# Optimization experiments

Measured on AMD Instinct MI355X. Metric: run time of the kernel, lower is better.

The kernel has to match this reference:

```python
import jax, jax.numpy as jnp
import numpy as np

N, E = 50000, 800000
SD, VD = 128, 16        # node scalar / vector channels
ESD, EVD = 32, 1        # edge scalar / vector channels
LN_EPS = 1e-5
VN_EPS = 1e-8


def setup_inputs():
    key = jax.random.key(0)
    ks = jax.random.split(key, 24)
    g = lambda i, shape, scale=0.05: jax.random.normal(ks[i], shape, dtype=jnp.float32) * scale
    inp = dict(
        node_s=jax.random.normal(ks[0], (N, SD), dtype=jnp.float32),
        node_v=jax.random.normal(ks[1], (N, VD, 3), dtype=jnp.float32),
        edge_index=jax.random.randint(ks[2], (2, E), 0, N, dtype=jnp.int32),
        edge_s=jax.random.normal(ks[3], (E, ESD), dtype=jnp.float32),
        edge_v=jax.random.normal(ks[4], (E, EVD, 3), dtype=jnp.float32),
        # LayerNorm (scalar channel) params
        ln_g=jnp.ones((SD,), jnp.float32), ln_b=jnp.zeros((SD,), jnp.float32),
        # edge_gvp: (ESD,EVD) -> (SD,VD)
        wes=g(5, (SD, ESD)), bes=jnp.zeros((SD,), jnp.float32),
        wev=g(6, (VD * 3, EVD * 3)), bev=jnp.zeros((VD * 3,), jnp.float32),
        # node_gvp: (SD,VD) -> (SD,VD)
        wns=g(7, (SD, SD)), bns=jnp.zeros((SD,), jnp.float32),
        wnv=g(8, (VD * 3, VD * 3)), bnv=jnp.zeros((VD * 3,), jnp.float32),
        # residual linears
        wrs=g(9, (SD, SD)), brs=jnp.zeros((SD,), jnp.float32),
        wrv=g(10, (VD * 3, VD * 3)), brv=jnp.zeros((VD * 3,), jnp.float32),
    )
    return inp


def _gvp(s, v, ws, bs, wv, bv, vo, scalar_act=True):
    """GVP with activations=(silu, None), vector_gate=True (faithful to source:
    fc_v acts on flattened [vi*3] coords)."""
    s_out = s @ ws.T + bs
    if scalar_act:
        s_out = jax.nn.silu(s_out)
    v_flat = v.reshape(v.shape[0], -1)                    # [*, vi*3]
    v_out = (v_flat @ wv.T + bv).reshape(v.shape[0], vo, 3)
    gate = jax.nn.sigmoid(s_out[..., :vo])
    v_out = v_out * gate[..., None]
    return s_out, v_out


def reference(node_s, node_v, edge_index, edge_s, edge_v,
              ln_g, ln_b, wes, bes, wev, bev, wns, bns, wnv, bnv,
              wrs, brs, wrv, brv):
    n = node_s.shape[0]
    # --- GVP LayerNorm (norm_first) ---
    mu = jnp.mean(node_s, axis=-1, keepdims=True)
    var = jnp.mean(jnp.square(node_s - mu), axis=-1, keepdims=True)
    s_n = (node_s - mu) * jax.lax.rsqrt(var + LN_EPS) * ln_g + ln_b
    vn2 = jnp.sum(jnp.square(node_v), axis=-1, keepdims=True)      # [N,VD,1]
    vnorm = jnp.sqrt(jnp.mean(vn2, axis=-2, keepdims=True) + VN_EPS)  # [N,1,1]
    v_n = node_v / vnorm

    # --- edge GVP ---
    ec_s, ec_v = _gvp(edge_s, edge_v, wes, bes, wev, bev, VD)      # [E,SD],[E,VD,3]

    # --- scatter-mean over destination nodes (nodes w/o incoming stay zero) ---
    dst = edge_index[1]
    cnt = jax.ops.segment_sum(jnp.ones((dst.shape[0],), ec_s.dtype), dst, num_segments=n)
    denom = jnp.maximum(cnt, 1.0)
    agg_s = jax.ops.segment_sum(ec_s, dst, num_segments=n) / denom[:, None]
    agg_v = jax.ops.segment_sum(ec_v, dst, num_segments=n) / denom[:, None, None]

    # --- node GVP on (normalized + aggregated) ---
    out_s, out_v = _gvp(s_n + agg_s, v_n + agg_v, wns, bns, wnv, bnv, VD)

    # --- residual linears (on normalized inputs; dropout = identity in eval) ---
    res_s = s_n @ wrs.T + brs
    res_v = (v_n.reshape(n, -1) @ wrv.T + brv).reshape(n, VD, 3)
    return out_s + res_s, out_v + res_v
```

## Files before the change

kernel.cpp:

```cpp
#include <hip/hip_runtime.h>

__device__ __forceinline__ float sigmoidf_(float x){ return 1.f/(1.f+__expf(-x)); }

__global__ void hist_kernel(const int* __restrict__ dst, int* __restrict__ cnt, int E){
  int e = blockIdx.x*blockDim.x + threadIdx.x;
  if (e < E) atomicAdd(&cnt[dst[e]], 1);
}

__global__ __launch_bounds__(1024) void scan_kernel(const int* __restrict__ cnt,
                                                    int* __restrict__ off,
                                                    int* __restrict__ wptr, int N){
  __shared__ int part[1024];
  const int t = threadIdx.x;
  const int chunk = (N + 1023) / 1024;
  const int lo = min(t*chunk, N), hi = min(lo+chunk, N);
  int s = 0;
  for (int i = lo; i < hi; i++) s += cnt[i];
  part[t] = s;
  __syncthreads();
  for (int o = 1; o < 1024; o <<= 1){
    int v = (t >= o) ? part[t-o] : 0;
    __syncthreads();
    part[t] += v;
    __syncthreads();
  }
  int run = part[t] - s;
  for (int i = lo; i < hi; i++){
    int c = cnt[i];
    off[i] = run; wptr[i] = run;
    run += c;
  }
  if (t == 1023) off[N] = part[1023];
}

__global__ void scatter_kernel(const int* __restrict__ dst, int* __restrict__ wptr,
                               int* __restrict__ csr, int E){
  int e = blockIdx.x*blockDim.x + threadIdx.x;
  if (e < E){
    int pos = atomicAdd(&wptr[dst[e]], 1);
    csr[pos] = e;
  }
}

__global__ __launch_bounds__(128) void edge_agg_kernel(
    const float* __restrict__ edge_s, const float* __restrict__ edge_v,
    const int* __restrict__ csr, const int* __restrict__ off,
    const float* __restrict__ wes, const float* __restrict__ bes,
    const float* __restrict__ wev, const float* __restrict__ bev,
    float* __restrict__ aggS, float* __restrict__ aggV, int N)
{
  const int t = threadIdx.x;
  float w[32];
  #pragma unroll
  for (int k = 0; k < 32; k += 4){
    float4 u = *(const float4*)(wes + t*32 + k);
    w[k]=u.x; w[k+1]=u.y; w[k+2]=u.z; w[k+3]=u.w;
  }
  const float bt = bes[t];
  const bool w0 = (t < 64);
  float wv0=0.f, wv1=0.f, wv2=0.f, bv=0.f;
  if (t < 48){ wv0=wev[t*3]; wv1=wev[t*3+1]; wv2=wev[t*3+2]; bv=bev[t]; }

  const int i = blockIdx.x;
  if (i >= N) return;
  const int jb = off[i], je = off[i+1];

  float accS = 0.f, accV = 0.f;
  if (jb < je){
    int e = csr[jb];
    float4 cur[8];
    {
      const float4* pr = (const float4*)(edge_s + (size_t)e*32);
      #pragma unroll
      for (int q = 0; q < 8; q++) cur[q] = pr[q];
    }
    float vx=0.f, vy=0.f, vz=0.f;
    if (w0){ const float* pv = edge_v + (size_t)e*3; vx=pv[0]; vy=pv[1]; vz=pv[2]; }

    for (int j = jb; j < je; j++){
      const int en = (j+1 < je) ? csr[j+1] : e;
      float4 nxt[8];
      {
        const float4* pn = (const float4*)(edge_s + (size_t)en*32);
        #pragma unroll
        for (int q = 0; q < 8; q++) nxt[q] = pn[q];
      }
      float nx=0.f, ny=0.f, nz=0.f;
      if (w0){ const float* pv = edge_v + (size_t)en*3; nx=pv[0]; ny=pv[1]; nz=pv[2]; }

      float d0 = 0.f, d1 = 0.f;
      #pragma unroll
      for (int q = 0; q < 8; q += 2){
        d0 += cur[q].x*w[4*q+0] + cur[q].y*w[4*q+1] + cur[q].z*w[4*q+2] + cur[q].w*w[4*q+3];
        d1 += cur[q+1].x*w[4*q+4] + cur[q+1].y*w[4*q+5] + cur[q+1].z*w[4*q+6] + cur[q+1].w*w[4*q+7];
      }
      const float acc = bt + d0 + d1;
      const float sil = acc * sigmoidf_(acc);
      accS += sil;
      if (w0){
        float g = __shfl(sil, (t < 48) ? (t/3) : 0, 64);
        if (t < 48) accV += (bv + wv0*vx + wv1*vy + wv2*vz) * sigmoidf_(g);
      }
      #pragma unroll
      for (int q = 0; q < 8; q++) cur[q] = nxt[q];
      vx=nx; vy=ny; vz=nz;
    }
  }
  const float rdn = 1.f / (float)max(je - jb, 1);
  aggS[(size_t)i*128 + t] = accS * rdn;
  if (t < 48) aggV[(size_t)i*48 + t] = accV * rdn;
}

#define NS_RS 68
#define NS_GS 17

__global__ __launch_bounds__(512, 4) void node_kernel(
    const float* __restrict__ node_s, const float* __restrict__ node_v,
    const float* __restrict__ ln_g, const float* __restrict__ ln_b,
    const float* __restrict__ wns, const float* __restrict__ bns,
    const float* __restrict__ wnv, const float* __restrict__ bnv,
    const float* __restrict__ wrs, const float* __restrict__ brs,
    const float* __restrict__ wrv, const float* __restrict__ brv,
    const float* __restrict__ aggS, const float* __restrict__ aggV,
    float* __restrict__ out_s, float* __restrict__ out_v, int N)
{
  __shared__ float shX[64*NS_RS];
  __shared__ float shS[64*NS_RS];
  __shared__ float shP1[128], shP2[128];
  __shared__ float shGate[64*NS_GS];

  const int tid  = threadIdx.x;
  const int lane = tid & 63;
  const int wv   = __builtin_amdgcn_readfirstlane(tid >> 6);
  const int i0   = blockIdx.x * 64;
  const int node = i0 + lane;

  if (wv < 2){
    float s1 = 0.f, s2 = 0.f;
    if (node < N){
      const float4* p = (const float4*)(node_s + (size_t)node*128 + wv*64);
      #pragma unroll
      for (int q = 0; q < 16; q++){
        const float4 v = p[q];
        s1 += (v.x+v.y)+(v.z+v.w);
        s2 += (v.x*v.x+v.y*v.y)+(v.z*v.z+v.w*v.w);
      }
    }
    shP1[wv*64+lane] = s1;
    shP2[wv*64+lane] = s2;
  }
  __syncthreads();

  float acc1[16], acc2[16];
  #pragma unroll
  for (int j = 0; j < 16; j++){ acc1[j]=0.f; acc2[j]=0.f; }
  const int cb = wv*16;

  for (int half = 0; half < 2; half++){
    const int kb = half*64;
    {
      const int n  = tid >> 3;
      const int kk = (tid & 7)*8;
      const int gn = i0 + n;
      const float s1 = shP1[n] + shP1[64+n];
      const float s2 = shP2[n] + shP2[64+n];
      const float m  = s1 * (1.f/128.f);
      const float r  = rsqrtf(s2*(1.f/128.f) - m*m + 1e-5f);
      float4 x0 = make_float4(0.f,0.f,0.f,0.f), x1 = x0, a0 = x0, a1v = x0;
      if (gn < N){
        const float4* ps = (const float4*)(node_s + (size_t)gn*128 + kb + kk);
        x0 = ps[0]; x1 = ps[1];
        const float4* pa = (const float4*)(aggS + (size_t)gn*128 + kb + kk);
        a0 = pa[0]; a1v = pa[1];
      }
      const float4 g0 = *(const float4*)(ln_g + kb + kk);
      const float4 g1 = *(const float4*)(ln_g + kb + kk + 4);
      const float4 b0 = *(const float4*)(ln_b + kb + kk);
      const float4 b1 = *(const float4*)(ln_b + kb + kk + 4);
      const float sn0 = (x0.x-m)*r*g0.x + b0.x;
      const float sn1 = (x0.y-m)*r*g0.y + b0.y;
      const float sn2 = (x0.z-m)*r*g0.z + b0.z;
      const float sn3 = (x0.w-m)*r*g0.w + b0.w;
      const float sn4 = (x1.x-m)*r*g1.x + b1.x;
      const float sn5 = (x1.y-m)*r*g1.y + b1.y;
      const float sn6 = (x1.z-m)*r*g1.z + b1.z;
      const float sn7 = (x1.w-m)*r*g1.w + b1.w;
      float* pS = &shS[n*NS_RS + kk];
      float* pX = &shX[n*NS_RS + kk];
      ((float4*)pS)[0] = make_float4(sn0,sn1,sn2,sn3);
      ((float4*)pS)[1] = make_float4(sn4,sn5,sn6,sn7);
      ((float4*)pX)[0] = make_float4(sn0+a0.x, sn1+a0.y, sn2+a0.z, sn3+a0.w);
      ((float4*)pX)[1] = make_float4(sn4+a1v.x, sn5+a1v.y, sn6+a1v.z, sn7+a1v.w);
    }
    __syncthreads();

    for (int kc = 0; kc < 64; kc += 8){
      const float4 xa = ((const float4*)&shX[lane*NS_RS + kc])[0];
      const float4 xb = ((const float4*)&shX[lane*NS_RS + kc])[1];
      const float4 sa = ((const float4*)&shS[lane*NS_RS + kc])[0];
      const float4 sb = ((const float4*)&shS[lane*NS_RS + kc])[1];
      #pragma unroll
      for (int j = 0; j < 16; j++){
        const float* w1 = wns + (size_t)(cb+j)*128 + kb + kc;
        const float* w2 = wrs + (size_t)(cb+j)*128 + kb + kc;
        const float4 u0 = ((const float4*)w1)[0], u1 = ((const float4*)w1)[1];
        const float4 y0 = ((const float4*)w2)[0], y1 = ((const float4*)w2)[1];
        acc1[j] += (xa.x*u0.x + xa.y*u0.y + xa.z*u0.z + xa.w*u0.w)
                 + (xb.x*u1.x + xb.y*u1.y + xb.z*u1.z + xb.w*u1.w);
        acc2[j] += (sa.x*y0.x + sa.y*y0.y + sa.z*y0.z + sa.w*y0.w)
                 + (sb.x*y1.x + sb.y*y1.y + sb.z*y1.z + sb.w*y1.w);
      }
    }
    __syncthreads();
  }

  {
    float o[16];
    #pragma unroll
    for (int j = 0; j < 16; j++){
      const float aa = acc1[j] + bns[cb+j];
      const float so = aa * sigmoidf_(aa);
      if (wv == 0) shGate[lane*NS_GS + j] = sigmoidf_(so);
      o[j] = so + acc2[j] + brs[cb+j];
    }
    if (node < N){
      float4* po = (float4*)(out_s + (size_t)node*128 + cb);
      #pragma unroll
      for (int q = 0; q < 4; q++)
        po[q] = make_float4(o[4*q],o[4*q+1],o[4*q+2],o[4*q+3]);
    }
  }
  __syncthreads();

  {
    const int vb = wv*6;
    float sv[48];
    float s3 = 0.f;
    if (node < N){
      const float4* pv = (const float4*)(node_v + (size_t)node*48);
      #pragma unroll
      for (int q = 0; q < 12; q++){
        const float4 v = pv[q];
        sv[4*q]=v.x; sv[4*q+1]=v.y; sv[4*q+2]=v.z; sv[4*q+3]=v.w;
        s3 += (v.x*v.x+v.y*v.y)+(v.z*v.z+v.w*v.w);
      }
    } else {
      #pragma unroll
      for (int k = 0; k < 48; k++) sv[k]=0.f;
    }
    const float rvn = rsqrtf(s3*(1.f/16.f) + 1e-8f);
    #pragma unroll
    for (int k = 0; k < 48; k++) sv[k] *= rvn;

    float a1[6], a2[6];
    #pragma unroll
    for (int j = 0; j < 6; j++){ a1[j]=0.f; a2[j]=0.f; }

    #pragma unroll
    for (int kc = 0; kc < 48; kc += 8){
      float xv[8];
      if (node < N){
        const float4* pa = (const float4*)(aggV + (size_t)node*48 + kc);
        const float4 av0 = pa[0], av1 = pa[1];
        xv[0]=sv[kc]+av0.x;   xv[1]=sv[kc+1]+av0.y;
        xv[2]=sv[kc+2]+av0.z; xv[3]=sv[kc+3]+av0.w;
        xv[4]=sv[kc+4]+av1.x; xv[5]=sv[kc+5]+av1.y;
        xv[6]=sv[kc+6]+av1.z; xv[7]=sv[kc+7]+av1.w;
      } else {
        #pragma unroll
        for (int q = 0; q < 8; q++) xv[q] = 0.f;
      }
      #pragma unroll
      for (int j = 0; j < 6; j++){
        const float* w1 = wnv + (size_t)(vb+j)*48 + kc;
        const float* w2 = wrv + (size_t)(vb+j)*48 + kc;
        const float4 u0 = ((const float4*)w1)[0], u1 = ((const float4*)w1)[1];
        const float4 y0 = ((const float4*)w2)[0], y1 = ((const float4*)w2)[1];
        a1[j] += (xv[0]*u0.x + xv[1]*u0.y + xv[2]*u0.z + xv[3]*u0.w)
               + (xv[4]*u1.x + xv[5]*u1.y + xv[6]*u1.z + xv[7]*u1.w);
        a2[j] += (sv[kc]*y0.x + sv[kc+1]*y0.y + sv[kc+2]*y0.z + sv[kc+3]*y0.w)
               + (sv[kc+4]*y1.x + sv[kc+5]*y1.y + sv[kc+6]*y1.z + sv[kc+7]*y1.w);
      }
    }
    if (node < N){
      const float g0 = shGate[lane*NS_GS + 2*wv];
      const float g1 = shGate[lane*NS_GS + 2*wv + 1];
      float ov[6];
      #pragma unroll
      for (int j = 0; j < 6; j++){
        const float g = (j < 3) ? g0 : g1;
        ov[j] = (a1[j] + bnv[vb+j])*g + a2[j] + brv[vb+j];
      }
      float2* po = (float2*)(out_v + (size_t)node*48 + vb);
      po[0] = make_float2(ov[0], ov[1]);
      po[1] = make_float2(ov[2], ov[3]);
      po[2] = make_float2(ov[4], ov[5]);
    }
  }
}

extern "C" void kernel_launch(void* const* d_in, const int* in_sizes, int n_in,
                              void* d_out, int out_size, void* d_ws, size_t ws_size,
                              hipStream_t stream)
{
  const float* node_s = (const float*)d_in[0];
  const float* node_v = (const float*)d_in[1];
  const int*   eidx   = (const int*)  d_in[2];
  const float* edge_s = (const float*)d_in[3];
  const float* edge_v = (const float*)d_in[4];
  const float* ln_g   = (const float*)d_in[5];
  const float* ln_b   = (const float*)d_in[6];
  const float* wes    = (const float*)d_in[7];
  const float* bes    = (const float*)d_in[8];
  const float* wev    = (const float*)d_in[9];
  const float* bev    = (const float*)d_in[10];
  const float* wns    = (const float*)d_in[11];
  const float* bns    = (const float*)d_in[12];
  const float* wnv    = (const float*)d_in[13];
  const float* bnv    = (const float*)d_in[14];
  const float* wrs    = (const float*)d_in[15];
  const float* brs    = (const float*)d_in[16];
  const float* wrv    = (const float*)d_in[17];
  const float* brv    = (const float*)d_in[18];

  const int N = in_sizes[0] / 128;
  const int E = in_sizes[3] / 32;
  const int* dst = eidx + E;

  float* aggS = (float*)d_ws;
  float* aggV = aggS + (size_t)N*128;

  int* off  = (int*)d_out;
  int* wptr = off + (N + 1);
  int* csr  = wptr + N;

  hipMemsetAsync(wptr, 0, (size_t)N*sizeof(int), stream);
  hist_kernel<<<(E+255)/256, 256, 0, stream>>>(dst, wptr, E);
  scan_kernel<<<1, 1024, 0, stream>>>(wptr, off, wptr, N);
  scatter_kernel<<<(E+255)/256, 256, 0, stream>>>(dst, wptr, csr, E);

  edge_agg_kernel<<<N, 128, 0, stream>>>(edge_s, edge_v, csr, off,
                                         wes, bes, wev, bev, aggS, aggV, N);

  float* out_s = (float*)d_out;
  float* out_v = out_s + (size_t)N*128;
  node_kernel<<<(N+63)/64, 512, 0, stream>>>(node_s, node_v, ln_g, ln_b,
                                             wns, bns, wnv, bnv,
                                             wrs, brs, wrv, brv,
                                             aggS, aggV, out_s, out_v, N);
}
```

Measured before the change: 822.4 us.

## Split edge GVP into edge-parallel kernel plus separate CSR segment aggregation

Computes the edge GVP with one thread per edge in CSR order, writing per-edge scalar and vector outputs to a workspace, then aggregates them per node in a separate kernel. This is meant to replace the serial per-node edge loop, which has low parallelism and is latency bound. In exchange it writes and reads a large intermediate buffer. The fallback fused kernel also drops its manual prefetch and gets launch bounds for occupancy.

```diff
diff --git a/kernel.cpp b/kernel.cpp
--- a/kernel.cpp
+++ b/kernel.cpp
@@ -42,7 +42,126 @@
   }
 }
 
-__global__ __launch_bounds__(128) void edge_agg_kernel(
+__global__ __launch_bounds__(256) void edge_gvp_kernel(
+    const float* __restrict__ edge_s, const float* __restrict__ edge_v,
+    const int* __restrict__ csr,
+    const float* __restrict__ wes, const float* __restrict__ bes,
+    const float* __restrict__ wev, const float* __restrict__ bev,
+    float* __restrict__ ecS, float* __restrict__ ecV, int E)
+{
+  __shared__ float shT[256*17];
+  const int t = threadIdx.x;
+  const int p0 = blockIdx.x*256;
+  const int p  = p0 + t;
+  const bool act = (p < E);
+
+  int e = 0;
+  if (act) e = csr[p];
+
+  float es[32];
+  if (act){
+    #pragma unroll
+    for (int k = 0; k < 32; k += 4){
+      float4 u = *(const float4*)(edge_s + (size_t)e*32 + k);
+      es[k]=u.x; es[k+1]=u.y; es[k+2]=u.z; es[k+3]=u.w;
+    }
+  } else {
+    #pragma unroll
+    for (int k = 0; k < 32; k++) es[k]=0.f;
+  }
+  float ev0=0.f, ev1=0.f, ev2=0.f;
+  if (act){
+    const float* pv = edge_v + (size_t)e*3;
+    ev0 = pv[0]; ev1 = pv[1]; ev2 = pv[2];
+  }
+
+  float gate[16];
+
+  for (int cb = 0; cb < 128; cb += 16){
+    float acc[16];
+    #pragma unroll
+    for (int c = 0; c < 16; c++){
+      float a = bes[cb+c];
+      const float* wr = wes + (size_t)(cb+c)*32;
+      #pragma unroll
+      for (int k = 0; k < 32; k++) a += es[k]*wr[k];
+      acc[c] = a * sigmoidf_(a);
+    }
+    if (cb == 0){
+      #pragma unroll
+      for (int c = 0; c < 16; c++) gate[c] = sigmoidf_(acc[c]);
+    }
+    __syncthreads();
+    #pragma unroll
+    for (int c = 0; c < 16; c += 4)
+      *(float4*)&shT[t*17 + c] = make_float4(acc[c],acc[c+1],acc[c+2],acc[c+3]);
+    __syncthreads();
+    #pragma unroll
+    for (int q = 0; q < 4; q++){
+      const int flat = q*256 + t;
+      const int row  = flat >> 2;
+      const int col  = (flat & 3)*4;
+      if (p0 + row < E){
+        const float* ps = &shT[row*17 + col];
+        *(float4*)(ecS + (size_t)(p0+row)*128 + cb + col) =
+          make_float4(ps[0], ps[1], ps[2], ps[3]);
+      }
+    }
+  }
+
+  for (int vb = 0; vb < 48; vb += 16){
+    float vo[16];
+    #pragma unroll
+    for (int cc = 0; cc < 16; cc++){
+      const int c = vb + cc;
+      vo[cc] = (bev[c] + wev[c*3]*ev0 + wev[c*3+1]*ev1 + wev[c*3+2]*ev2)
+               * gate[c/3];
+    }
+    __syncthreads();
+    #pragma unroll
+    for (int c = 0; c < 16; c += 4)
+      *(float4*)&shT[t*17 + c] = make_float4(vo[c],vo[c+1],vo[c+2],vo[c+3]);
+    __syncthreads();
+    #pragma unroll
+    for (int q = 0; q < 4; q++){
+      const int flat = q*256 + t;
+      const int row  = flat >> 2;
+      const int col  = (flat & 3)*4;
+      if (p0 + row < E){
+        const float* ps = &shT[row*17 + col];
+        *(float4*)(ecV + (size_t)(p0+row)*48 + vb + col) =
+          make_float4(ps[0], ps[1], ps[2], ps[3]);
+      }
+    }
+  }
+}
+
+#define AGG_NB 16
+__global__ __launch_bounds__(192) void agg_kernel(
+    const float* __restrict__ ecS, const float* __restrict__ ecV,
+    const int* __restrict__ off,
+    float* __restrict__ aggS, float* __restrict__ aggV, int N)
+{
+  const int t = threadIdx.x;
+  const int i0 = blockIdx.x*AGG_NB;
+  const int i1 = min(i0 + AGG_NB, N);
+  for (int i = i0; i < i1; i++){
+    const int jb = off[i], je = off[i+1];
+    const float rdn = 1.f / (float)max(je - jb, 1);
+    if (t < 128){
+      float a = 0.f;
+      for (int j = jb; j < je; j++) a += ecS[(size_t)j*128 + t];
+      aggS[(size_t)i*128 + t] = a * rdn;
+    } else if (t < 176){
+      const int c = t - 128;
+      float a = 0.f;
+      for (int j = jb; j < je; j++) a += ecV[(size_t)j*48 + c];
+      aggV[(size_t)i*48 + c] = a * rdn;
+    }
+  }
+}
+
+__global__ __launch_bounds__(128, 3) void edge_agg_kernel(
     const float* __restrict__ edge_s, const float* __restrict__ edge_v,
     const int* __restrict__ csr, const int* __restrict__ off,
     const float* __restrict__ wes, const float* __restrict__ bes,
@@ -57,53 +176,34 @@
     w[k]=u.x; w[k+1]=u.y; w[k+2]=u.z; w[k+3]=u.w;
   }
   const float bt = bes[t];
-  const bool w0 = (t < 64);
   float wv0=0.f, wv1=0.f, wv2=0.f, bv=0.f;
   if (t < 48){ wv0=wev[t*3]; wv1=wev[t*3+1]; wv2=wev[t*3+2]; bv=bev[t]; }
 
   const int i = blockIdx.x;
   if (i >= N) return;
-  const int jb = off[i], je = off[i+1];
+  const int jb = __builtin_amdgcn_readfirstlane(off[i]);
+  const int je = __builtin_amdgcn_readfirstlane(off[i+1]);
 
   float accS = 0.f, accV = 0.f;
-  if (jb < je){
-    int e = csr[jb];
-    float4 cur[8];
-    {
-      const float4* pr = (const float4*)(edge_s + (size_t)e*32);
-      #pragma unroll
-      for (int q = 0; q < 8; q++) cur[q] = pr[q];
-    }
-    float vx=0.f, vy=0.f, vz=0.f;
-    if (w0){ const float* pv = edge_v + (size_t)e*3; vx=pv[0]; vy=pv[1]; vz=pv[2]; }
-
-    for (int j = jb; j < je; j++){
-      const int en = (j+1 < je) ? csr[j+1] : e;
-      float4 nxt[8];
-      {
-        const float4* pn = (const float4*)(edge_s + (size_t)en*32);
-        #pragma unroll
-        for (int q = 0; q < 8; q++) nxt[q] = pn[q];
-      }
-      float nx=0.f, ny=0.f, nz=0.f;
-      if (w0){ const float* pv = edge_v + (size_t)en*3; nx=pv[0]; ny=pv[1]; nz=pv[2]; }
-
-      float d0 = 0.f, d1 = 0.f;
-      #pragma unroll
-      for (int q = 0; q < 8; q += 2){
-        d0 += cur[q].x*w[4*q+0] + cur[q].y*w[4*q+1] + cur[q].z*w[4*q+2] + cur[q].w*w[4*q+3];
-        d1 += cur[q+1].x*w[4*q+4] + cur[q+1].y*w[4*q+5] + cur[q+1].z*w[4*q+6] + cur[q+1].w*w[4*q+7];
-      }
-      const float acc = bt + d0 + d1;
-      const float sil = acc * sigmoidf_(acc);
-      accS += sil;
-      if (w0){
-        float g = __shfl(sil, (t < 48) ? (t/3) : 0, 64);
-        if (t < 48) accV += (bv + wv0*vx + wv1*vy + wv2*vz) * sigmoidf_(g);
-      }
-      #pragma unroll
-      for (int q = 0; q < 8; q++) cur[q] = nxt[q];
-      vx=nx; vy=ny; vz=nz;
+  for (int j = jb; j < je; j++){
+    const int e_ = csr[j];
+    const float4* pr = (const float4*)(edge_s + (size_t)e_*32);
+    float d0 = 0.f, d1 = 0.f;
+    #pragma unroll
+    for (int q = 0; q < 8; q += 2){
+      float4 r0 = pr[q], r1 = pr[q+1];
+      d0 += r0.x*w[4*q+0] + r0.y*w[4*q+1] + r0.z*w[4*q+2] + r0.w*w[4*q+3];
+      d1 += r1.x*w[4*q+4] + r1.y*w[4*q+5] + r1.z*w[4*q+6] + r1.w*w[4*q+7];
+    }
+    const float acc = bt + d0 + d1;
+    const float sil = acc * sigmoidf_(acc);
+    accS += sil;
+    if (t < 64){
+      float ex=0.f, ey=0.f, ez=0.f;
+      const float* pv = edge_v + (size_t)e_*3;
+      ex = pv[0]; ey = pv[1]; ez = pv[2];
+      const float g = __shfl(sil, t/3, 64);
+      if (t < 48) accV += (bv + wv0*ex + wv1*ey + wv2*ez) * sigmoidf_(g);
     }
   }
   const float rdn = 1.f / (float)max(je - jb, 1);
@@ -329,6 +429,9 @@
 
   float* aggS = (float*)d_ws;
   float* aggV = aggS + (size_t)N*128;
+  float* ecS  = aggS + (size_t)N*176;
+  float* ecV  = ecS  + (size_t)E*128;
+  const size_t need = ((size_t)N*176 + (size_t)E*176) * sizeof(float);
 
   int* off  = (int*)d_out;
   int* wptr = off + (N + 1);
@@ -339,8 +442,16 @@
   scan_kernel<<<1, 1024, 0, stream>>>(wptr, off, wptr, N);
   scatter_kernel<<<(E+255)/256, 256, 0, stream>>>(dst, wptr, csr, E);
 
-  edge_agg_kernel<<<N, 128, 0, stream>>>(edge_s, edge_v, csr, off,
-                                         wes, bes, wev, bev, aggS, aggV, N);
+  if (ws_size >= need){
+    edge_gvp_kernel<<<(E+255)/256, 256, 0, stream>>>(edge_s, edge_v, csr,
+                                                     wes, bes, wev, bev,
+                                                     ecS, ecV, E);
+    agg_kernel<<<(N+AGG_NB-1)/AGG_NB, 192, 0, stream>>>(ecS, ecV, off,
+                                                        aggS, aggV, N);
+  } else {
+    edge_agg_kernel<<<N, 128, 0, stream>>>(edge_s, edge_v, csr, off,
+                                           wes, bes, wev, bev, aggS, aggV, N);
+  }
 
   float* out_s = (float*)d_out;
   float* out_v = out_s + (size_t)N*128;
```

Result: slower. 843.1 us (+2.5%).

## Switch edge aggregation to edge-parallel blocks with in-block segmented reduction

Applied to the files above, without the earlier changes.

Replaces the one-block-per-node edge GVP aggregation with an edge-parallel kernel. Each thread processes one CSR-sorted edge, computes all 128 scalar and 48 vector outputs, and writes them through shared memory. Runs of equal destination nodes are then reduced in-block, with atomics only for runs that span block boundaries. This removes the per-node serial loop and load imbalance from degree variation. In exchange it adds an extra node-id array, a memset of the aggregation buffers, heavy per-thread weight reads from global memory, and more block syncs.

```diff
diff --git a/kernel.cpp b/kernel.cpp
--- a/kernel.cpp
+++ b/kernel.cpp
@@ -34,81 +34,135 @@
 }
 
 __global__ void scatter_kernel(const int* __restrict__ dst, int* __restrict__ wptr,
-                               int* __restrict__ csr, int E){
+                               int* __restrict__ csr, int* __restrict__ node2, int E){
   int e = blockIdx.x*blockDim.x + threadIdx.x;
   if (e < E){
-    int pos = atomicAdd(&wptr[dst[e]], 1);
+    int d = dst[e];
+    int pos = atomicAdd(&wptr[d], 1);
     csr[pos] = e;
-  }
-}
-
-__global__ __launch_bounds__(128) void edge_agg_kernel(
+    node2[pos] = d;
+  }
+}
+
+__global__ __launch_bounds__(256) void edge_agg2_kernel(
     const float* __restrict__ edge_s, const float* __restrict__ edge_v,
-    const int* __restrict__ csr, const int* __restrict__ off,
+    const int* __restrict__ csr, const int* __restrict__ node2,
+    const int* __restrict__ off,
     const float* __restrict__ wes, const float* __restrict__ bes,
     const float* __restrict__ wev, const float* __restrict__ bev,
-    float* __restrict__ aggS, float* __restrict__ aggV, int N)
+    float* __restrict__ aggS, float* __restrict__ aggV, int E)
 {
-  const int t = threadIdx.x;
-  float w[32];
+  __shared__ float shT[256*17];
+  __shared__ int   shNid[256];
+  __shared__ int   shRunStart[258];
+  __shared__ int   shRunNode[257];
+  __shared__ int   shWaveCnt[4];
+  __shared__ int   shNumRuns, shActCnt;
+
+  const int t  = threadIdx.x;
+  const int wv = t >> 6, ln = t & 63;
+  const int p0 = blockIdx.x * 256;
+  const int p  = p0 + t;
+  const bool act = (p < E);
+
+  int e = 0, nid = -1;
+  if (act){ e = csr[p]; nid = node2[p]; }
+
+  float es[32];
+  float ev0 = 0.f, ev1 = 0.f, ev2 = 0.f;
+  if (act){
+    #pragma unroll
+    for (int k = 0; k < 32; k += 4){
+      float4 u = *(const float4*)(edge_s + (size_t)e*32 + k);
+      es[k]=u.x; es[k+1]=u.y; es[k+2]=u.z; es[k+3]=u.w;
+    }
+    const float* pv = edge_v + (size_t)e*3;
+    ev0 = pv[0]; ev1 = pv[1]; ev2 = pv[2];
+  } else {
+    #pragma unroll
+    for (int k = 0; k < 32; k++) es[k] = 0.f;
+  }
+
+  shNid[t] = nid;
+  __syncthreads();
+  const int prevN = (t == 0) ? -2 : shNid[t-1];
+  const bool flag = act && (nid != prevN);
+  const unsigned long long bal = __ballot(flag);
+  if (ln == 0) shWaveCnt[wv] = __popcll(bal);
+  __syncthreads();
+  if (t == 0){
+    int s = 0;
+    #pragma unroll
+    for (int k = 0; k < 4; k++){ int c = shWaveCnt[k]; shWaveCnt[k] = s; s += c; }
+    shNumRuns = s;
+    shActCnt  = min(E - p0, 256);
+  }
+  __syncthreads();
+  const int numRuns = shNumRuns;
+  if (flag){
+    const int rid = shWaveCnt[wv] + __popcll(bal & ((1ull<<ln) - 1ull));
+    shRunStart[rid] = t;
+    shRunNode[rid]  = nid;
+  }
+  if (t == 0) shRunStart[numRuns] = shActCnt;
+  __syncthreads();
+
+#define REDUCE_STORE(BASE, STRIDE, CHBASE)                                    \
+  for (int r = (t >> 4); r < numRuns; r += 16){                               \
+    const int c  = t & 15;                                                    \
+    const int s0 = shRunStart[r], s1 = shRunStart[r+1];                       \
+    const int nd = shRunNode[r];                                              \
+    float sum = 0.f;                                                          \
+    for (int j = s0; j < s1; j++) sum += shT[j*17 + c];                       \
+    if (r == 0 || r == numRuns-1){                                            \
+      const int deg = off[nd+1] - off[nd];                                    \
+      atomicAdd(BASE + (size_t)nd*STRIDE + (CHBASE) + c,                      \
+                sum * (1.f/(float)deg));                                      \
+    } else {                                                                  \
+      BASE[(size_t)nd*STRIDE + (CHBASE) + c] = sum * (1.f/(float)(s1 - s0));  \
+    }                                                                         \
+  }
+
+  float g16[16];
+  for (int cb = 0; cb < 128; cb += 16){
+    float acc[16];
+    #pragma unroll
+    for (int c = 0; c < 16; c++){
+      float a = bes[cb+c];
+      const float* wr = wes + (size_t)(cb+c)*32;
+      #pragma unroll
+      for (int k = 0; k < 32; k++) a += es[k]*wr[k];
+      acc[c] = a * sigmoidf_(a);
+    }
+    if (cb == 0){
+      #pragma unroll
+      for (int c = 0; c < 16; c++) g16[c] = sigmoidf_(acc[c]);
+    }
+    __syncthreads();
+    #pragma unroll
+    for (int c = 0; c < 16; c += 4)
+      *(float4*)&shT[t*17 + c] = make_float4(acc[c],acc[c+1],acc[c+2],acc[c+3]);
+    __syncthreads();
+    REDUCE_STORE(aggS, 128, cb)
+  }
+
   #pragma unroll
-  for (int k = 0; k < 32; k += 4){
-    float4 u = *(const float4*)(wes + t*32 + k);
-    w[k]=u.x; w[k+1]=u.y; w[k+2]=u.z; w[k+3]=u.w;
-  }
-  const float bt = bes[t];
-  const bool w0 = (t < 64);
-  float wv0=0.f, wv1=0.f, wv2=0.f, bv=0.f;
-  if (t < 48){ wv0=wev[t*3]; wv1=wev[t*3+1]; wv2=wev[t*3+2]; bv=bev[t]; }
-
-  const int i = blockIdx.x;
-  if (i >= N) return;
-  const int jb = off[i], je = off[i+1];
-
-  float accS = 0.f, accV = 0.f;
-  if (jb < je){
-    int e = csr[jb];
-    float4 cur[8];
-    {
-      const float4* pr = (const float4*)(edge_s + (size_t)e*32);
-      #pragma unroll
-      for (int q = 0; q < 8; q++) cur[q] = pr[q];
-    }
-    float vx=0.f, vy=0.f, vz=0.f;
-    if (w0){ const float* pv = edge_v + (size_t)e*3; vx=pv[0]; vy=pv[1]; vz=pv[2]; }
-
-    for (int j = jb; j < je; j++){
-      const int en = (j+1 < je) ? csr[j+1] : e;
-      float4 nxt[8];
-      {
-        const float4* pn = (const float4*)(edge_s + (size_t)en*32);
-        #pragma unroll
-        for (int q = 0; q < 8; q++) nxt[q] = pn[q];
-      }
-      float nx=0.f, ny=0.f, nz=0.f;
-      if (w0){ const float* pv = edge_v + (size_t)en*3; nx=pv[0]; ny=pv[1]; nz=pv[2]; }
-
-      float d0 = 0.f, d1 = 0.f;
-      #pragma unroll
-      for (int q = 0; q < 8; q += 2){
-        d0 += cur[q].x*w[4*q+0] + cur[q].y*w[4*q+1] + cur[q].z*w[4*q+2] + cur[q].w*w[4*q+3];
-        d1 += cur[q+1].x*w[4*q+4] + cur[q+1].y*w[4*q+5] + cur[q+1].z*w[4*q+6] + cur[q+1].w*w[4*q+7];
-      }
-      const float acc = bt + d0 + d1;
-      const float sil = acc * sigmoidf_(acc);
-      accS += sil;
-      if (w0){
-        float g = __shfl(sil, (t < 48) ? (t/3) : 0, 64);
-        if (t < 48) accV += (bv + wv0*vx + wv1*vy + wv2*vz) * sigmoidf_(g);
-      }
-      #pragma unroll
-      for (int q = 0; q < 8; q++) cur[q] = nxt[q];
-      vx=nx; vy=ny; vz=nz;
-    }
-  }
-  const float rdn = 1.f / (float)max(je - jb, 1);
-  aggS[(size_t)i*128 + t] = accS * rdn;
-  if (t < 48) aggV[(size_t)i*48 + t] = accV * rdn;
+  for (int vb = 0; vb < 48; vb += 16){
+    float vo[16];
+    #pragma unroll
+    for (int cc = 0; cc < 16; cc++){
+      const int c = vb + cc;
+      vo[cc] = (bev[c] + wev[c*3]*ev0 + wev[c*3+1]*ev1 + wev[c*3+2]*ev2)
+               * g16[c/3];
+    }
+    __syncthreads();
+    #pragma unroll
+    for (int c = 0; c < 16; c += 4)
+      *(float4*)&shT[t*17 + c] = make_float4(vo[c],vo[c+1],vo[c+2],vo[c+3]);
+    __syncthreads();
+    REDUCE_STORE(aggV, 48, vb)
+  }
+#undef REDUCE_STORE
 }
 
 #define NS_RS 68
@@ -330,17 +384,20 @@
   float* aggS = (float*)d_ws;
   float* aggV = aggS + (size_t)N*128;
 
-  int* off  = (int*)d_out;
-  int* wptr = off + (N + 1);
-  int* csr  = wptr + N;
+  int* off   = (int*)d_out;
+  int* wptr  = off + (N + 1);
+  int* csr   = wptr + N;
+  int* node2 = csr + E;
 
   hipMemsetAsync(wptr, 0, (size_t)N*sizeof(int), stream);
+  hipMemsetAsync(aggS, 0, (size_t)N*176*sizeof(float), stream);
   hist_kernel<<<(E+255)/256, 256, 0, stream>>>(dst, wptr, E);
   scan_kernel<<<1, 1024, 0, stream>>>(wptr, off, wptr, N);
-  scatter_kernel<<<(E+255)/256, 256, 0, stream>>>(dst, wptr, csr, E);
-
-  edge_agg_kernel<<<N, 128, 0, stream>>>(edge_s, edge_v, csr, off,
-                                         wes, bes, wev, bev, aggS, aggV, N);
+  scatter_kernel<<<(E+255)/256, 256, 0, stream>>>(dst, wptr, csr, node2, E);
+
+  edge_agg2_kernel<<<(E+255)/256, 256, 0, stream>>>(edge_s, edge_v, csr, node2, off,
+                                                    wes, bes, wev, bev,
+                                                    aggS, aggV, E);
 
   float* out_s = (float*)d_out;
   float* out_v = out_s + (size_t)N*128;
```

After: 777.8 us. -5.4%, faster.
